# Optimization experiments

Hardware: AMD Instinct MI355X
Metric: run time of the kernel (lower is better)

Reference implementation:

```python
import jax, jax.numpy as jnp
import numpy as np

OUT_FEATURES = 4096
IN_FEATURES = 4096
NNZ = 838860
N_COLS = 8192


def setup_inputs() -> dict:
    key = jax.random.key(0)
    k_r, k_c, k_v, k_x = jax.random.split(key, 4)
    rows = jax.random.randint(k_r, (NNZ,), 0, OUT_FEATURES, dtype=jnp.int32)
    cols = jax.random.randint(k_c, (NNZ,), 0, IN_FEATURES, dtype=jnp.int32)
    vals = jax.random.normal(k_v, (NNZ,), dtype=jnp.float32)
    x = jax.random.normal(k_x, (IN_FEATURES, N_COLS), dtype=jnp.float32)
    return {"rows": rows, "cols": cols, "vals": vals, "x": x}


def reference(rows, cols, vals, x):
    # Sparse COO weight W[out, in]; duplicate (row, col) entries sum, matching
    # uncoalesced COO semantics of torch.sparse.mm.
    # Dense scatter + GEMM is the clean, efficient jax expression of the same math.
    W = jnp.zeros((OUT_FEATURES, IN_FEATURES), dtype=vals.dtype).at[rows, cols].add(vals)
    return W @ x  # [out_features, N]
```

## Files before the change

### kernel.cpp

```cpp
#include <hip/hip_runtime.h>

#define OUT_F 4096
#define IN_F  4096
#define NCOLS 8192

#define GM OUT_F
#define GK IN_F
#define GN NCOLS

typedef __attribute__((ext_vector_type(8))) short short8;
typedef __attribute__((ext_vector_type(4))) float f32x4;

__device__ inline unsigned short f2bf(float f) {
    union { float f; unsigned u; } c; c.f = f;
    unsigned u = c.u;
    u += 0x7fffu + ((u >> 16) & 1u);
    return (unsigned short)(u >> 16);
}

__device__ inline void gll16(const void* g, void* l) {
    __builtin_amdgcn_global_load_lds(
        (const __attribute__((address_space(1))) unsigned int*)g,
        (__attribute__((address_space(3))) unsigned int*)l, 16, 0, 0);
}

__global__ void scatter_dense(const int* __restrict__ rows, const int* __restrict__ cols,
                              const float* __restrict__ vals, float* __restrict__ W, int nnz) {
    int i = blockIdx.x * blockDim.x + threadIdx.x;
    if (i < nnz) atomicAdd(&W[(size_t)rows[i] * IN_F + cols[i]], vals[i]);
}

__global__ void convert_w(const float* __restrict__ Wf, unsigned short* __restrict__ Wb) {
    int i = blockIdx.x * blockDim.x + threadIdx.x;
    float4 v = ((const float4*)Wf)[i];
    ushort4 o;
    o.x = f2bf(v.x); o.y = f2bf(v.y); o.z = f2bf(v.z); o.w = f2bf(v.w);
    ((ushort4*)Wb)[i] = o;
}

__global__ __launch_bounds__(256) void transpose_x(const float* __restrict__ x,
                                                   unsigned short* __restrict__ xT) {
    __shared__ float tile[64][65];
    const int k0 = blockIdx.x * 64;
    const int n0 = blockIdx.y * 64;
    const int t = threadIdx.x;
    const int c4 = (t & 15) * 4;
    const int r0 = t >> 4;
    for (int p = 0; p < 4; ++p) {
        int r = r0 + p * 16;
        float4 v = *(const float4*)&x[(size_t)(k0 + r) * NCOLS + n0 + c4];
        tile[r][c4 + 0] = v.x; tile[r][c4 + 1] = v.y;
        tile[r][c4 + 2] = v.z; tile[r][c4 + 3] = v.w;
    }
    __syncthreads();
    const int n  = t >> 2;
    const int ks = (t & 3) * 16;
    unsigned w[8];
    for (int m = 0; m < 8; ++m) {
        unsigned short lo = f2bf(tile[ks + 2 * m + 0][n]);
        unsigned short hi = f2bf(tile[ks + 2 * m + 1][n]);
        w[m] = (unsigned)lo | ((unsigned)hi << 16);
    }
    uint4* dst = (uint4*)&xT[(size_t)(n0 + n) * GK + k0 + ks];
    dst[0] = make_uint4(w[0], w[1], w[2], w[3]);
    dst[1] = make_uint4(w[4], w[5], w[6], w[7]);
}

__global__ __launch_bounds__(512, 2) void gemm256(const unsigned short* __restrict__ A,
                                                  const unsigned short* __restrict__ BT,
                                                  float* __restrict__ C) {
    __shared__ unsigned short lds[65536];

    const int tid  = threadIdx.x;
    const int wave = tid >> 6;
    const int lane = tid & 63;

    const int wg   = blockIdx.y * 32 + blockIdx.x;
    const int xcd  = wg & 7;
    const int ii   = wg >> 3;
    const int m0   = ((((ii & 7) << 1) | (xcd & 1))) << 8;
    const int n0   = ((((ii >> 3) << 2) | ((xcd >> 1) & 3))) << 8;
    const int wm = wave >> 2;
    const int wn = wave & 3;

    const int r0s  = tid >> 2;
    const int swz0 = ((tid & 3) ^ ((r0s >> 1) & 3)) << 3;
    const unsigned short* pA0 = A  + (size_t)(m0 + r0s) * GK + swz0;
    const unsigned short* pA1 = pA0 + (size_t)128 * GK;
    const unsigned short* pB0 = BT + (size_t)(n0 + r0s) * GK + swz0;
    const unsigned short* pB1 = pB0 + (size_t)128 * GK;

    const int frow  = lane & 15;
    const int ajb   = ((lane >> 4) ^ ((frow >> 1) & 3)) << 3;
    const int abase = (((wm << 7) + frow) << 5) + ajb;
    const int bbase = (((wn << 6) + frow) << 5) + 8192 + ajb;

    f32x4 acc[8][4] = {};

#define STAGE(T_, s_) do {                                              \
        const int ko_ = ((T_) & 127) << 5;                              \
        gll16(pA0 + ko_, &lds[(s_) * 16384 + (wave << 9)]);             \
        gll16(pA1 + ko_, &lds[(s_) * 16384 + 4096 + (wave << 9)]);      \
        gll16(pB0 + ko_, &lds[(s_) * 16384 + 8192 + (wave << 9)]);      \
        gll16(pB1 + ko_, &lds[(s_) * 16384 + 12288 + (wave << 9)]);     \
    } while (0)

    STAGE(0, 0); STAGE(1, 1); STAGE(2, 2);
    asm volatile("s_waitcnt vmcnt(8)");
    __builtin_amdgcn_s_barrier();

#define PHASE(e_, jj) do {                                                      \
        const unsigned short* Ar = &lds[(e_) * 16384];                          \
        short8 bf[4], af[4], af2[4];                                            \
        _Pragma("unroll")                                                       \
        for (int nj = 0; nj < 4; ++nj)                                          \
            bf[nj] = *(const short8*)&Ar[bbase + nj * 512];                     \
        _Pragma("unroll")                                                       \
        for (int mi = 0; mi < 4; ++mi)                                          \
            af[mi] = *(const short8*)&Ar[abase + mi * 512];                     \
        _Pragma("unroll")                                                       \
        for (int mi = 0; mi < 4; ++mi)                                          \
            af2[mi] = *(const short8*)&Ar[abase + 2048 + mi * 512];             \
        STAGE(4 * (jj) + (e_) + 3, ((e_) + 3) & 3);                             \
        asm volatile("s_waitcnt vmcnt(8)");                                     \
        __builtin_amdgcn_s_barrier();                                           \
        __builtin_amdgcn_s_setprio(1);                                          \
        _Pragma("unroll")                                                       \
        for (int mi = 0; mi < 4; ++mi)                                          \
            _Pragma("unroll")                                                   \
            for (int nj = 0; nj < 4; ++nj)                                      \
                acc[mi][nj] = __builtin_amdgcn_mfma_f32_16x16x32_bf16(          \
                    af[mi], bf[nj], acc[mi][nj], 0, 0, 0);                      \
        _Pragma("unroll")                                                       \
        for (int mi = 0; mi < 4; ++mi)                                          \
            _Pragma("unroll")                                                   \
            for (int nj = 0; nj < 4; ++nj)                                      \
                acc[4 + mi][nj] = __builtin_amdgcn_mfma_f32_16x16x32_bf16(      \
                    af2[mi], bf[nj], acc[4 + mi][nj], 0, 0, 0);                 \
        __builtin_amdgcn_s_setprio(0);                                          \
        __builtin_amdgcn_s_barrier();                                           \
    } while (0)

#pragma unroll 1
    for (int j = 0; j < GK / 128; ++j) {
        PHASE(0, j);
        PHASE(1, j);
        PHASE(2, j);
        PHASE(3, j);
    }
#undef PHASE
#undef STAGE

    for (int mi = 0; mi < 8; ++mi) {
        const int r0w = m0 + wm * 128 + mi * 16 + (lane >> 4) * 4;
        for (int nj = 0; nj < 4; ++nj) {
            const int cc = n0 + wn * 64 + nj * 16 + frow;
            for (int r = 0; r < 4; ++r)
                C[(size_t)(r0w + r) * GN + cc] = acc[mi][nj][r];
        }
    }
}

#define WS_COUNTS  0
#define WS_OFFSETS 4097
#define WS_CURSOR  8194
#define WS_HEADER  12290

__global__ void hist_kernel(const int* __restrict__ rows, int* __restrict__ counts, int nnz) {
    int i = blockIdx.x * blockDim.x + threadIdx.x;
    if (i < nnz) atomicAdd(&counts[rows[i]], 1);
}

__global__ void scan_kernel(const int* __restrict__ counts, int* __restrict__ offsets) {
    __shared__ int lsum[256];
    int t = threadIdx.x;
    int base = t * 16;
    int local[16];
    int s = 0;
    for (int i = 0; i < 16; ++i) { local[i] = counts[base + i]; s += local[i]; }
    lsum[t] = s;
    __syncthreads();
    if (t == 0) {
        int acc = 0;
        for (int i = 0; i < 256; ++i) { int v = lsum[i]; lsum[i] = acc; acc += v; }
        offsets[OUT_F] = acc;
    }
    __syncthreads();
    int acc = lsum[t];
    for (int i = 0; i < 16; ++i) { offsets[base + i] = acc; acc += local[i]; }
}

__global__ void scatter_kernel(const int* __restrict__ rows, const int* __restrict__ cols,
                               const float* __restrict__ vals,
                               const int* __restrict__ offsets, int* __restrict__ cursor,
                               int* __restrict__ cols_s, float* __restrict__ vals_s, int nnz) {
    int i = blockIdx.x * blockDim.x + threadIdx.x;
    if (i < nnz) {
        int r = rows[i];
        int pos = offsets[r] + atomicAdd(&cursor[r], 1);
        cols_s[pos] = cols[i];
        vals_s[pos] = vals[i];
    }
}

__global__ __launch_bounds__(256) void spmm_kernel(const int* __restrict__ offsets,
                                                   const int* __restrict__ cols_s,
                                                   const float* __restrict__ vals_s,
                                                   const float* __restrict__ x,
                                                   float* __restrict__ out) {
    const int row  = blockIdx.x;
    const int col0 = blockIdx.y * 1024 + threadIdx.x * 4;
    const int k0 = offsets[row];
    const int k1 = offsets[row + 1];
    float4 acc = make_float4(0.f, 0.f, 0.f, 0.f);
    for (int k = k0; k < k1; ++k) {
        const int   c = cols_s[k];
        const float v = vals_s[k];
        const float4 xv = *reinterpret_cast<const float4*>(x + (size_t)c * NCOLS + col0);
        acc.x += v * xv.x;
        acc.y += v * xv.y;
        acc.z += v * xv.z;
        acc.w += v * xv.w;
    }
    *reinterpret_cast<float4*>(out + (size_t)row * NCOLS + col0) = acc;
}

extern "C" void kernel_launch(void* const* d_in, const int* in_sizes, int n_in,
                              void* d_out, int out_size, void* d_ws, size_t ws_size,
                              hipStream_t stream) {
    const int*   rows = (const int*)d_in[0];
    const int*   cols = (const int*)d_in[1];
    const float* vals = (const float*)d_in[2];
    const float* x    = (const float*)d_in[3];
    float*       out  = (float*)d_out;
    const int nnz = in_sizes[0];

    const size_t WF_BYTES = (size_t)GM * GK * 4;
    const size_t WB_BYTES = (size_t)GM * GK * 2;
    const size_t NEED = WF_BYTES + WB_BYTES;

    if (ws_size >= NEED) {
        float*          Wf = (float*)d_ws;
        unsigned short* Wb = (unsigned short*)((char*)d_ws + WF_BYTES);
        unsigned short* xT = (unsigned short*)d_ws;

        hipMemsetAsync(Wf, 0, WF_BYTES, stream);
        scatter_dense<<<(nnz + 255) / 256, 256, 0, stream>>>(rows, cols, vals, Wf, nnz);
        convert_w<<<(GM * GK / 4) / 256, 256, 0, stream>>>(Wf, Wb);
        dim3 tg(GK / 64, GN / 64);
        transpose_x<<<tg, 256, 0, stream>>>(x, xT);
        dim3 gg(GN / 256, GM / 256);
        gemm256<<<gg, 512, 0, stream>>>(Wb, xT, out);
    } else {
        int*   ws_i    = (int*)d_ws;
        int*   counts  = ws_i + WS_COUNTS;
        int*   offsets = ws_i + WS_OFFSETS;
        int*   cursor  = ws_i + WS_CURSOR;
        int*   cols_s  = ws_i + WS_HEADER;
        float* vals_s  = (float*)(ws_i + WS_HEADER + nnz);

        hipMemsetAsync(d_ws, 0, (size_t)WS_HEADER * sizeof(int), stream);
        const int nblk = (nnz + 255) / 256;
        hist_kernel<<<nblk, 256, 0, stream>>>(rows, counts, nnz);
        scan_kernel<<<1, 256, 0, stream>>>(counts, offsets);
        scatter_kernel<<<nblk, 256, 0, stream>>>(rows, cols, vals, offsets, cursor,
                                                 cols_s, vals_s, nnz);
        dim3 grid(OUT_F, NCOLS / 1024);
        spmm_kernel<<<grid, 256, 0, stream>>>(offsets, cols_s, vals_s, x, out);
    }
}
```

Before: 501.7 us.

## Prefetch next-stage LDS fragments into double-buffered registers and drop trailing barrier

Restructures the GEMM main loop so each phase loads the next stage's A/B fragments from LDS into alternating register sets while the current stage's MFMAs run. Only one barrier per phase remains, and the vmcnt wait becomes vmcnt(4). The aim is to hide LDS read latency behind MFMA work and cut barrier stalls. In exchange it raises register pressure, and the removed barrier risks a race: the STAGE write into buffer (e+3)&3 can overlap other waves still reading that buffer.

```diff
diff --git a/kernel.cpp b/kernel.cpp
--- a/kernel.cpp
+++ b/kernel.cpp
@@ -109,44 +109,55 @@
     asm volatile("s_waitcnt vmcnt(8)");
     __builtin_amdgcn_s_barrier();
 
-#define PHASE(e_, jj) do {                                                      \
-        const unsigned short* Ar = &lds[(e_) * 16384];                          \
-        short8 bf[4], af[4], af2[4];                                            \
+    short8 bfX[4], afX[4], bfY[4], afY[4];
+    {
+        const unsigned short* Ar0 = &lds[0];
+#pragma unroll
+        for (int nj = 0; nj < 4; ++nj) bfX[nj] = *(const short8*)&Ar0[bbase + nj * 512];
+#pragma unroll
+        for (int mi = 0; mi < 4; ++mi) afX[mi] = *(const short8*)&Ar0[abase + mi * 512];
+    }
+
+#define PHASE(e_, bfC, afC, bfN, afN, jj) do {                                  \
+        asm volatile("s_waitcnt vmcnt(4)");                                     \
+        __builtin_amdgcn_s_barrier();                                           \
+        __builtin_amdgcn_sched_barrier(0);                                      \
+        const unsigned short* ArC = &lds[(e_) * 16384];                         \
+        const unsigned short* ArN = &lds[(((e_) + 1) & 3) * 16384];             \
+        short8 af2[4];                                                          \
+        _Pragma("unroll")                                                       \
+        for (int mi = 0; mi < 4; ++mi)                                          \
+            af2[mi] = *(const short8*)&ArC[abase + 2048 + mi * 512];            \
         _Pragma("unroll")                                                       \
         for (int nj = 0; nj < 4; ++nj)                                          \
-            bf[nj] = *(const short8*)&Ar[bbase + nj * 512];                     \
-        _Pragma("unroll")                                                       \
-        for (int mi = 0; mi < 4; ++mi)                                          \
-            af[mi] = *(const short8*)&Ar[abase + mi * 512];                     \
-        _Pragma("unroll")                                                       \
-        for (int mi = 0; mi < 4; ++mi)                                          \
-            af2[mi] = *(const short8*)&Ar[abase + 2048 + mi * 512];             \
+            bfN[nj] = *(const short8*)&ArN[bbase + nj * 512];                   \
+        _Pragma("unroll")                                                       \
+        for (int mi = 0; mi < 4; ++mi)                                          \
+            afN[mi] = *(const short8*)&ArN[abase + mi * 512];                   \
         STAGE(4 * (jj) + (e_) + 3, ((e_) + 3) & 3);                             \
-        asm volatile("s_waitcnt vmcnt(8)");                                     \
-        __builtin_amdgcn_s_barrier();                                           \
+        __builtin_amdgcn_sched_barrier(0);                                      \
         __builtin_amdgcn_s_setprio(1);                                          \
         _Pragma("unroll")                                                       \
         for (int mi = 0; mi < 4; ++mi)                                          \
             _Pragma("unroll")                                                   \
             for (int nj = 0; nj < 4; ++nj)                                      \
                 acc[mi][nj] = __builtin_amdgcn_mfma_f32_16x16x32_bf16(          \
-                    af[mi], bf[nj], acc[mi][nj], 0, 0, 0);                      \
+                    afC[mi], bfC[nj], acc[mi][nj], 0, 0, 0);                    \
         _Pragma("unroll")                                                       \
         for (int mi = 0; mi < 4; ++mi)                                          \
             _Pragma("unroll")                                                   \
             for (int nj = 0; nj < 4; ++nj)                                      \
                 acc[4 + mi][nj] = __builtin_amdgcn_mfma_f32_16x16x32_bf16(      \
-                    af2[mi], bf[nj], acc[4 + mi][nj], 0, 0, 0);                 \
+                    af2[mi], bfC[nj], acc[4 + mi][nj], 0, 0, 0);                \
         __builtin_amdgcn_s_setprio(0);                                          \
-        __builtin_amdgcn_s_barrier();                                           \
     } while (0)
 
 #pragma unroll 1
     for (int j = 0; j < GK / 128; ++j) {
-        PHASE(0, j);
-        PHASE(1, j);
-        PHASE(2, j);
-        PHASE(3, j);
+        PHASE(0, bfX, afX, bfY, afY, j);
+        PHASE(1, bfY, afY, bfX, afX, j);
+        PHASE(2, bfX, afX, bfY, afY, j);
+        PHASE(3, bfY, afY, bfX, afX, j);
     }
 #undef PHASE
 #undef STAGE
```

Measured after the change: 484.6 us. -3.4%, faster.
